# Performance work log

Hardware: AMD Instinct MI355X
Metric: run time of the kernel (lower is better)

The kernel has to match this reference:

```python
import jax, jax.numpy as jnp
import numpy as np

B, S, HID = 2, 2048, 2048
H, HK, D = 32, 8, 64
N_REP = H // HK
SCALE = D ** -0.5


def setup_inputs() -> dict:
    key = jax.random.key(0)
    ks = jax.random.split(key, 9)
    std = HID ** -0.5
    causal = jnp.tril(jnp.ones((S, S), dtype=bool))
    attention_mask = jnp.where(causal, 0.0, -1e9).astype(jnp.float32)[None, None]  # [1,1,S,S]
    return {
        "hidden_states": jax.random.normal(ks[0], (B, S, HID), jnp.float32),
        "attention_mask": attention_mask,
        "q_w": jax.random.normal(ks[1], (HID, H * D), jnp.float32) * std,
        "q_b": jax.random.normal(ks[2], (H * D,), jnp.float32) * 0.01,
        "k_w": jax.random.normal(ks[3], (HID, HK * D), jnp.float32) * std,
        "k_b": jax.random.normal(ks[4], (HK * D,), jnp.float32) * 0.01,
        "v_w": jax.random.normal(ks[5], (HID, HK * D), jnp.float32) * std,
        "v_b": jax.random.normal(ks[6], (HK * D,), jnp.float32) * 0.01,
        "dense_w": jax.random.normal(ks[7], (HID, HID), jnp.float32) * std,
        "dense_b": jax.random.normal(ks[8], (HID,), jnp.float32) * 0.01,
    }


def reference(hidden_states, attention_mask, q_w, q_b, k_w, k_b, v_w, v_b, dense_w, dense_b):
    b, s, _ = hidden_states.shape
    # projections -> [b, h, s, d]
    q = (hidden_states @ q_w + q_b).reshape(b, s, H, D).transpose(0, 2, 1, 3)
    k = (hidden_states @ k_w + k_b).reshape(b, s, HK, D).transpose(0, 2, 1, 3)
    v = (hidden_states @ v_w + v_b).reshape(b, s, HK, D).transpose(0, 2, 1, 3)
    # GQA: repeat_kv (repeat_interleave along head dim)
    k = jnp.repeat(k, N_REP, axis=1)  # [b, H, s, d]
    v = jnp.repeat(v, N_REP, axis=1)
    # eager attention: full score matrix
    scores = jnp.einsum("bhqd,bhkd->bhqk", q, k) * SCALE + attention_mask
    w = jax.nn.softmax(scores.astype(jnp.float32), axis=-1).astype(q.dtype)
    attn = jnp.einsum("bhqk,bhkd->bhqd", w, v)
    attn = attn.transpose(0, 2, 1, 3).reshape(b, s, H * D)
    return attn @ dense_w + dense_b
```

## Files before the change

### kernel.cpp

```cpp
#include <hip/hip_runtime.h>
#include <hip/hip_bf16.h>


typedef short s16x8 __attribute__((ext_vector_type(8)));
typedef float f32x4 __attribute__((ext_vector_type(4)));

static constexpr int BB = 2, SS = 2048, HID = 2048, HH = 32, HKV = 8, DD = 64;
static constexpr int MM = BB * SS;
static constexpr int NQKV = 3072;

#define DEV __device__ __forceinline__

DEV short f2bf(float f) {
    unsigned u = __builtin_bit_cast(unsigned, f);
    return (short)((u + 0x7fffu + ((u >> 16) & 1u)) >> 16);
}

DEV void stage16(const short* gsrc, short* lbase) {
    __builtin_amdgcn_global_load_lds((const __attribute__((address_space(1))) void*)gsrc,
                                     (__attribute__((address_space(3))) void*)lbase, 16, 0, 0);
}

__global__ __launch_bounds__(256) void cvt_f32_bf16(const float* __restrict__ in,
                                                    short* __restrict__ out, int n) {
    int i = (blockIdx.x * 256 + threadIdx.x) * 8;
    if (i >= n) return;
    float4 a = *reinterpret_cast<const float4*>(in + i);
    float4 b = *reinterpret_cast<const float4*>(in + i + 4);
    s16x8 o;
    o[0] = f2bf(a.x); o[1] = f2bf(a.y); o[2] = f2bf(a.z); o[3] = f2bf(a.w);
    o[4] = f2bf(b.x); o[5] = f2bf(b.y); o[6] = f2bf(b.z); o[7] = f2bf(b.w);
    *reinterpret_cast<s16x8*>(out + i) = o;
}

__global__ __launch_bounds__(256) void transpose_cvt(const float* __restrict__ in,
                                                     short* __restrict__ out,
                                                     int K, int N) {
    __shared__ float tile[32][33];
    int k0 = blockIdx.x * 32, n0 = blockIdx.y * 32;
    int tx = threadIdx.x & 31, ty = threadIdx.x >> 5;
#pragma unroll
    for (int r = ty; r < 32; r += 8)
        tile[r][tx] = in[(size_t)(k0 + r) * N + n0 + tx];
    __syncthreads();
#pragma unroll
    for (int r = ty; r < 32; r += 8)
        out[(size_t)(n0 + r) * K + k0 + tx] = f2bf(tile[tx][r]);
}

__global__ __launch_bounds__(256) void transpose_v(const short* __restrict__ QKV,
                                                   short* __restrict__ Vtg) {
    __shared__ int tile[32][33];
    const int s0 = blockIdx.x * 32, c0 = blockIdx.y * 32, b = blockIdx.z;
    const int tx = threadIdx.x & 31, ty = threadIdx.x >> 5;
#pragma unroll
    for (int r = ty; r < 32; r += 8)
        tile[r][tx] = QKV[(size_t)(b * SS + s0 + r) * NQKV + 2560 + c0 + tx];
    __syncthreads();
#pragma unroll
    for (int r = ty; r < 32; r += 8) {
        const int c = c0 + r;
        Vtg[((size_t)(b * HKV + (c >> 6)) * 64 + (c & 63)) * SS + s0 + tx] = (short)tile[tx][r];
    }
}

__global__ __launch_bounds__(256) void concat_bias(const float* __restrict__ qb,
                                                   const float* __restrict__ kb,
                                                   const float* __restrict__ vb,
                                                   float* __restrict__ cb) {
    int i = blockIdx.x * 256 + threadIdx.x;
    if (i < 2048) cb[i] = qb[i];
    else if (i < 2560) cb[i] = kb[i - 2048];
    else if (i < 3072) cb[i] = vb[i - 2560];
}

template <int BM, int BN, typename OutT>
__global__ __launch_bounds__(512) void gemm8p(const short* __restrict__ A,
                                              const short* __restrict__ Bt,
                                              const float* __restrict__ bias,
                                              OutT* __restrict__ C,
                                              int M, int N, int K, int qcols) {
    constexpr int NREP = BN / 64;
    constexpr int LA = BM / 128, LB = BN / 128;
    constexpr int W = LA + LB;
    __shared__ __align__(16) short lds[(BM + BN) * 128];
    const int tid = threadIdx.x, lane = tid & 63, wid = tid >> 6;
    const int fr = lane & 15, fk = lane >> 4;
    const int wm = wid >> 2, wn = wid & 3;
    const int nbn = N / BN;
    const int cpx = gridDim.x >> 3;
    const int wg = (blockIdx.x & 7) * cpx + (blockIdx.x >> 3);
    const int bm = wg / nbn, bn = wg % nbn;
    const int NT = K / 64;

    const short* Ablk = A + (size_t)bm * BM * K;
    const short* Bblk = Bt + (size_t)bn * BN * K;

    auto abase = [&](int bf, int kh) { return bf * (BM * 64) + kh * (BM * 32); };
    auto bbase = [&](int bf, int kh) { return 2 * (BM * 64) + bf * (BN * 64) + kh * (BN * 32); };

    auto stA = [&](int bf, int kh, int kt) {
#pragma unroll
        for (int l = 0; l < LA; ++l) {
            const int c = l * 512 + tid;
            const int r = c >> 2, sg = (c & 3) ^ ((r >> 1) & 3);
            stage16(Ablk + (size_t)r * K + kt + kh * 32 + sg * 8,
                    &lds[abase(bf, kh) + (l * 512 + wid * 64) * 8]);
        }
    };
    auto stB = [&](int bf, int kh, int kt) {
#pragma unroll
        for (int l = 0; l < LB; ++l) {
            const int c = l * 512 + tid;
            const int r = c >> 2, sg = (c & 3) ^ ((r >> 1) & 3);
            stage16(Bblk + (size_t)r * K + kt + kh * 32 + sg * 8,
                    &lds[bbase(bf, kh) + (l * 512 + wid * 64) * 8]);
        }
    };

    f32x4 acc[8][NREP] = {};

    stA(0, 0, 0); stB(0, 0, 0); stA(0, 1, 0); stB(0, 1, 0);
    asm volatile("s_waitcnt vmcnt(%0)" :: "n"(W) : "memory");
    __builtin_amdgcn_s_barrier();

    for (int t = 0; t < NT; ++t) {
        const int bf = t & 1, sf = bf ^ 1;
        const int ktn = (t + 1) * 64;
        const bool pf = (t + 1 < NT);
        s16x8 bfrag[NREP];
#pragma unroll
        for (int p = 0; p < 4; ++p) {
            const int ks = p >> 1, mh = p & 1;
            if (mh == 0) {
#pragma unroll
                for (int n = 0; n < NREP; ++n) {
                    const int row = wn * (BN / 4) + n * 16 + fr;
                    bfrag[n] = *reinterpret_cast<const s16x8*>(
                        &lds[bbase(bf, ks) + row * 32 + ((fk ^ ((row >> 1) & 3)) * 8)]);
                }
            }
            s16x8 afrag[4];
#pragma unroll
            for (int i = 0; i < 4; ++i) {
                const int row = wm * (BM / 2) + (mh * 4 + i) * 16 + fr;
                afrag[i] = *reinterpret_cast<const s16x8*>(
                    &lds[abase(bf, ks) + row * 32 + ((fk ^ ((row >> 1) & 3)) * 8)]);
            }
            if (pf) {
                if (p == 0) stA(sf, 0, ktn);
                else if (p == 1) stB(sf, 0, ktn);
                else if (p == 2) stA(sf, 1, ktn);
                else stB(sf, 1, ktn);
            }
            __builtin_amdgcn_s_barrier();
            asm volatile("s_waitcnt lgkmcnt(0)" ::: "memory");
            __builtin_amdgcn_sched_barrier(0);
            __builtin_amdgcn_s_setprio(1);
#pragma unroll
            for (int i = 0; i < 4; ++i)
#pragma unroll
                for (int n = 0; n < NREP; ++n)
                    acc[mh * 4 + i][n] = __builtin_amdgcn_mfma_f32_16x16x32_bf16(
                        afrag[i], bfrag[n], acc[mh * 4 + i][n], 0, 0, 0);
            __builtin_amdgcn_s_setprio(0);
            if (p == 1) {
                if (pf) asm volatile("s_waitcnt vmcnt(%0)" :: "n"(W) : "memory");
                else    asm volatile("s_waitcnt vmcnt(0)" ::: "memory");
            } else if (p == 3) {
                if (pf) asm volatile("s_waitcnt vmcnt(%0)" :: "n"(W) : "memory");
            }
            __builtin_amdgcn_s_barrier();
        }
    }

#pragma unroll
    for (int n = 0; n < NREP; ++n) {
        const int col = bn * BN + wn * (BN / 4) + n * 16 + fr;
        const float bv = bias[col];
        const float sc = (col < qcols) ? 0.125f : 1.0f;
#pragma unroll
        for (int mi = 0; mi < 8; ++mi) {
            const int row0 = bm * BM + wm * (BM / 2) + mi * 16 + fk * 4;
#pragma unroll
            for (int r = 0; r < 4; ++r) {
                const float v = (acc[mi][n][r] + bv) * sc;
                if constexpr (sizeof(OutT) == 2)
                    reinterpret_cast<short*>(C)[(size_t)(row0 + r) * N + col] = f2bf(v);
                else
                    reinterpret_cast<float*>(C)[(size_t)(row0 + r) * N + col] = v;
            }
        }
    }
}

__global__ __launch_bounds__(256, 2) void attn_fwd(
        const short* __restrict__ QKV,
        const short* __restrict__ Vtg,
        short* __restrict__ Ob) {
    constexpr int KB = 64;
    __shared__ __align__(16) short Qs[128 * 64];
    __shared__ __align__(16) short Ks[2][KB * 64];
    __shared__ __align__(16) short Vt[2][64 * 64];
    __shared__ __align__(16) short Ps[128 * 64];

    const int pair = blockIdx.x;
    const int bh = blockIdx.y;
    const int b = bh >> 5, h = bh & 31;
    const int kvh = h >> 2;
    const int tid = threadIdx.x, lane = tid & 63, wid = tid >> 6;
    const int fr = lane & 15, fk = lane >> 4;
    const int wq0 = wid * 32;

    const short* kbase = QKV + (size_t)b * SS * NQKV + 2048 + kvh * DD;
    const short* vbase = Vtg + (size_t)(b * HKV + kvh) * 64 * SS;

    auto stageKV = [&](int bb, int kv0) {
#pragma unroll
        for (int is = 0; is < 2; ++is) {
            const int c = is * 256 + wid * 64 + lane;
            const int r = c >> 3, sg = (c & 7) ^ (r & 7);
            stage16(kbase + (size_t)(kv0 + r) * NQKV + sg * 8,
                    &Ks[bb][(is * 256 + wid * 64) * 8]);
            stage16(vbase + (size_t)r * SS + kv0 + sg * 8,
                    &Vt[bb][(is * 256 + wid * 64) * 8]);
        }
    };
    auto stageQ = [&](int q0) {
        const short* qbase = QKV + ((size_t)b * SS + q0) * NQKV + h * DD;
#pragma unroll
        for (int is = 0; is < 4; ++is) {
            const int c = is * 256 + wid * 64 + lane;
            const int r = c >> 3, sg = (c & 7) ^ (r & 7);
            stage16(qbase + (size_t)r * NQKV + sg * 8,
                    &Qs[(is * 256 + wid * 64) * 8]);
        }
    };

    s16x8 ones = {};
    if (fr == 0) {
#pragma unroll
        for (int e = 0; e < 8; ++e) ones[e] = (short)0x3F80;
    }

    int cur = 0;
    stageQ(pair * 128);
    stageKV(0, 0);

    for (int sidx = 0; sidx < 2; ++sidx) {
        const int strip = sidx ? (15 - pair) : pair;
        const int q0 = strip * 128;
        const size_t qrow0 = (size_t)b * SS + q0;
        const int nt = 2 * strip + 2;

        __syncthreads();

        s16x8 aq[2][2];
#pragma unroll
        for (int i = 0; i < 2; ++i)
#pragma unroll
            for (int ks = 0; ks < 2; ++ks) {
                const int row = wq0 + i * 16 + fr;
                const int byte = (ks * 64 + fk * 16) ^ ((row & 7) << 4);
                aq[i][ks] = *reinterpret_cast<const s16x8*>(
                    reinterpret_cast<const char*>(Qs) + row * 128 + byte);
            }

        f32x4 acc_o[2][4] = {};
        f32x4 acc_l[2] = {};

        for (int t = 0; t < nt; ++t) {
            const int kv0 = t * KB;
            if (t + 1 < nt) {
                stageKV(cur ^ 1, kv0 + KB);
            } else if (sidx == 0) {
                stageQ((15 - pair) * 128);
                stageKV(cur ^ 1, 0);
            }

            f32x4 sacc[2][4] = {};
            __builtin_amdgcn_s_setprio(1);
#pragma unroll
            for (int j = 0; j < 4; ++j)
#pragma unroll
                for (int ks = 0; ks < 2; ++ks) {
                    const int row = j * 16 + fr;
                    const int byte = (ks * 64 + fk * 16) ^ ((row & 7) << 4);
                    s16x8 bk = *reinterpret_cast<const s16x8*>(
                        reinterpret_cast<const char*>(Ks[cur]) + row * 128 + byte);
#pragma unroll
                    for (int i = 0; i < 2; ++i)
                        sacc[i][j] = __builtin_amdgcn_mfma_f32_16x16x32_bf16(aq[i][ks], bk, sacc[i][j], 0, 0, 0);
                }
            __builtin_amdgcn_s_setprio(0);

            if (kv0 + KB - 1 > q0 + wq0) {
#pragma unroll
                for (int i = 0; i < 2; ++i) {
                    const int qg = q0 + wq0 + i * 16 + fk * 4;
#pragma unroll
                    for (int j = 0; j < 4; ++j) {
                        const int kvc = kv0 + j * 16 + fr;
#pragma unroll
                        for (int r = 0; r < 4; ++r)
                            if (kvc > qg + r) sacc[i][j][r] = -INFINITY;
                    }
                }
            }

#pragma unroll
            for (int i = 0; i < 2; ++i)
#pragma unroll
                for (int j = 0; j < 4; ++j)
#pragma unroll
                    for (int r = 0; r < 4; ++r) {
                        const int row = wq0 + i * 16 + fk * 4 + r;
                        const int byte = ((j * 16 + fr) * 2) ^ ((row & 7) << 4);
                        *reinterpret_cast<short*>(reinterpret_cast<char*>(Ps) + row * 128 + byte) =
                            f2bf(__expf(sacc[i][j][r]));
                    }

            s16x8 ap[2][2];
#pragma unroll
            for (int i = 0; i < 2; ++i)
#pragma unroll
                for (int ks = 0; ks < 2; ++ks) {
                    const int row = wq0 + i * 16 + fr;
                    const int byte = (ks * 64 + fk * 16) ^ ((row & 7) << 4);
                    ap[i][ks] = *reinterpret_cast<const s16x8*>(
                        reinterpret_cast<const char*>(Ps) + row * 128 + byte);
                }

            __builtin_amdgcn_s_setprio(1);
#pragma unroll
            for (int jd = 0; jd < 4; ++jd)
#pragma unroll
                for (int ks = 0; ks < 2; ++ks) {
                    const int row = jd * 16 + fr;
                    const int byte = (ks * 64 + fk * 16) ^ ((row & 7) << 4);
                    s16x8 bv = *reinterpret_cast<const s16x8*>(
                        reinterpret_cast<const char*>(Vt[cur]) + row * 128 + byte);
#pragma unroll
                    for (int i = 0; i < 2; ++i)
                        acc_o[i][jd] = __builtin_amdgcn_mfma_f32_16x16x32_bf16(ap[i][ks], bv, acc_o[i][jd], 0, 0, 0);
                }
#pragma unroll
            for (int i = 0; i < 2; ++i)
#pragma unroll
                for (int ks = 0; ks < 2; ++ks)
                    acc_l[i] = __builtin_amdgcn_mfma_f32_16x16x32_bf16(ap[i][ks], ones, acc_l[i], 0, 0, 0);
            __builtin_amdgcn_s_setprio(0);

            __syncthreads();
            cur ^= 1;
        }

#pragma unroll
        for (int i = 0; i < 2; ++i)
#pragma unroll
            for (int r = 0; r < 4; ++r) {
                const float l = __shfl(acc_l[i][r], (lane & 48));
                const float inv = 1.f / l;
                const size_t grow = (qrow0 + wq0 + i * 16 + fk * 4 + r) * (size_t)(HH * DD) + h * DD;
#pragma unroll
                for (int jd = 0; jd < 4; ++jd)
                    Ob[grow + jd * 16 + fr] = f2bf(acc_o[i][jd][r] * inv);
            }
    }
}

extern "C" void kernel_launch(void* const* d_in, const int* in_sizes, int n_in,
                              void* d_out, int out_size, void* d_ws, size_t ws_size,
                              hipStream_t stream) {
    const float* hidden  = (const float*)d_in[0];
    const float* q_w     = (const float*)d_in[2];
    const float* q_b     = (const float*)d_in[3];
    const float* k_w     = (const float*)d_in[4];
    const float* k_b     = (const float*)d_in[5];
    const float* v_w     = (const float*)d_in[6];
    const float* v_b     = (const float*)d_in[7];
    const float* dense_w = (const float*)d_in[8];
    const float* dense_b = (const float*)d_in[9];
    float* out = (float*)d_out;

    short* wt   = (short*)d_ws;
    short* dwt  = wt + 6291456;
    short* QKV  = dwt + 4194304;
    short* Vtg  = QKV + 12582912;
    short* hidb = Vtg + 2097152;
    short* Ob   = hidb;
    float* cbias = (float*)(hidb + 8388608);

    cvt_f32_bf16<<<4096, 256, 0, stream>>>(hidden, hidb, MM * HID);
    transpose_cvt<<<dim3(64, 64), 256, 0, stream>>>(q_w, wt, HID, HH * DD);
    transpose_cvt<<<dim3(64, 16), 256, 0, stream>>>(k_w, wt + 2048 * 2048, HID, HKV * DD);
    transpose_cvt<<<dim3(64, 16), 256, 0, stream>>>(v_w, wt + 2560 * 2048, HID, HKV * DD);
    transpose_cvt<<<dim3(64, 64), 256, 0, stream>>>(dense_w, dwt, HID, HID);
    concat_bias<<<12, 256, 0, stream>>>(q_b, k_b, v_b, cbias);

    gemm8p<256, 256, short><<<192, 512, 0, stream>>>(hidb, wt, cbias, QKV, MM, NQKV, HID, 2048);

    transpose_v<<<dim3(64, 16, 2), 256, 0, stream>>>(QKV, Vtg);

    attn_fwd<<<dim3(8, 64), 256, 0, stream>>>(QKV, Vtg, Ob);

    gemm8p<256, 128, float><<<256, 512, 0, stream>>>(Ob, dwt, dense_b, out, MM, HID, HID, 0);
}
```

Baseline: 199.2 us.

## Restructure GEMM pipeline to two phases per k-tile and retile QKV to 256x192

The GEMM main loop drops from four barrier-separated phases per k-tile to two. Each phase loads all 8 A fragments, interleaves the A and B prefetch issues between two MFMA halves, and uses per-wave vmcnt waits so it needs one barrier instead of two. The QKV projection switches from 256x256 tiles on 192 blocks to 256x192 tiles on 256 blocks to fill more CUs, so some threads issue an uneven number of B loads. This adds register pressure from holding 8 A fragments and relies on exact vmcnt bookkeeping for correctness.

Result: faster. 188.5 us (-5.4%).

```diff
diff --git a/kernel.cpp b/kernel.cpp
--- a/kernel.cpp
+++ b/kernel.cpp
@@ -80,9 +80,11 @@
                                               const float* __restrict__ bias,
                                               OutT* __restrict__ C,
                                               int M, int N, int K, int qcols) {
-    constexpr int NREP = BN / 64;
-    constexpr int LA = BM / 128, LB = BN / 128;
-    constexpr int W = LA + LB;
+    constexpr int NR = BN / 64;
+    constexpr int ACH = BM * 4;
+    constexpr int BCH = BN * 4;
+    static_assert(ACH % 512 == 0, "A chunks per half must be thread-uniform");
+    constexpr int SA = ACH / 512;
     __shared__ __align__(16) short lds[(BM + BN) * 128];
     const int tid = threadIdx.x, lane = tid & 63, wid = tid >> 6;
     const int fr = lane & 15, fk = lane >> 4;
@@ -101,7 +103,7 @@
 
     auto stA = [&](int bf, int kh, int kt) {
 #pragma unroll
-        for (int l = 0; l < LA; ++l) {
+        for (int l = 0; l < SA; ++l) {
             const int c = l * 512 + tid;
             const int r = c >> 2, sg = (c & 3) ^ ((r >> 1) & 3);
             stage16(Ablk + (size_t)r * K + kt + kh * 32 + sg * 8,
@@ -109,79 +111,89 @@
         }
     };
     auto stB = [&](int bf, int kh, int kt) {
-#pragma unroll
-        for (int l = 0; l < LB; ++l) {
-            const int c = l * 512 + tid;
+        {
+            const int c = tid;
             const int r = c >> 2, sg = (c & 3) ^ ((r >> 1) & 3);
             stage16(Bblk + (size_t)r * K + kt + kh * 32 + sg * 8,
-                    &lds[bbase(bf, kh) + (l * 512 + wid * 64) * 8]);
+                    &lds[bbase(bf, kh) + (wid * 64) * 8]);
+        }
+        if constexpr (BCH > 512) {
+            if (tid < BCH - 512) {
+                const int c = 512 + tid;
+                const int r = c >> 2, sg = (c & 3) ^ ((r >> 1) & 3);
+                stage16(Bblk + (size_t)r * K + kt + kh * 32 + sg * 8,
+                        &lds[bbase(bf, kh) + ((512 + wid * 64)) * 8]);
+            }
         }
     };
 
-    f32x4 acc[8][NREP] = {};
-
-    stA(0, 0, 0); stB(0, 0, 0); stA(0, 1, 0); stB(0, 1, 0);
-    asm volatile("s_waitcnt vmcnt(%0)" :: "n"(W) : "memory");
-    __builtin_amdgcn_s_barrier();
+    auto waithalf = [&](bool pf) {
+        if (!pf) { asm volatile("s_waitcnt vmcnt(0)" ::: "memory"); return; }
+        if constexpr (BCH > 512) {
+            if (wid < (BCH - 512) / 64) asm volatile("s_waitcnt vmcnt(4)" ::: "memory");
+            else                        asm volatile("s_waitcnt vmcnt(3)" ::: "memory");
+        } else {
+            asm volatile("s_waitcnt vmcnt(3)" ::: "memory");
+        }
+    };
+
+    f32x4 acc[8][NR] = {};
+
+    stA(0, 0, 0); stB(0, 0, 0);
+    stA(0, 1, 0); stB(0, 1, 0);
+    waithalf(true);
+    asm volatile("s_barrier" ::: "memory");
 
     for (int t = 0; t < NT; ++t) {
         const int bf = t & 1, sf = bf ^ 1;
         const int ktn = (t + 1) * 64;
         const bool pf = (t + 1 < NT);
-        s16x8 bfrag[NREP];
-#pragma unroll
-        for (int p = 0; p < 4; ++p) {
-            const int ks = p >> 1, mh = p & 1;
-            if (mh == 0) {
-#pragma unroll
-                for (int n = 0; n < NREP; ++n) {
-                    const int row = wn * (BN / 4) + n * 16 + fr;
-                    bfrag[n] = *reinterpret_cast<const s16x8*>(
-                        &lds[bbase(bf, ks) + row * 32 + ((fk ^ ((row >> 1) & 3)) * 8)]);
-                }
-            }
-            s16x8 afrag[4];
-#pragma unroll
-            for (int i = 0; i < 4; ++i) {
-                const int row = wm * (BM / 2) + (mh * 4 + i) * 16 + fr;
+#pragma unroll
+        for (int kh = 0; kh < 2; ++kh) {
+            s16x8 bfrag[NR], afrag[8];
+#pragma unroll
+            for (int n = 0; n < NR; ++n) {
+                const int row = wn * (BN / 4) + n * 16 + fr;
+                bfrag[n] = *reinterpret_cast<const s16x8*>(
+                    &lds[bbase(bf, kh) + row * 32 + ((fk ^ ((row >> 1) & 3)) * 8)]);
+            }
+#pragma unroll
+            for (int i = 0; i < 8; ++i) {
+                const int row = wm * 128 + i * 16 + fr;
                 afrag[i] = *reinterpret_cast<const s16x8*>(
-                    &lds[abase(bf, ks) + row * 32 + ((fk ^ ((row >> 1) & 3)) * 8)]);
-            }
-            if (pf) {
-                if (p == 0) stA(sf, 0, ktn);
-                else if (p == 1) stB(sf, 0, ktn);
-                else if (p == 2) stA(sf, 1, ktn);
-                else stB(sf, 1, ktn);
-            }
-            __builtin_amdgcn_s_barrier();
-            asm volatile("s_waitcnt lgkmcnt(0)" ::: "memory");
-            __builtin_amdgcn_sched_barrier(0);
+                    &lds[abase(bf, kh) + row * 32 + ((fk ^ ((row >> 1) & 3)) * 8)]);
+            }
+            if (pf) stA(sf, kh, ktn);
             __builtin_amdgcn_s_setprio(1);
 #pragma unroll
             for (int i = 0; i < 4; ++i)
 #pragma unroll
-                for (int n = 0; n < NREP; ++n)
-                    acc[mh * 4 + i][n] = __builtin_amdgcn_mfma_f32_16x16x32_bf16(
-                        afrag[i], bfrag[n], acc[mh * 4 + i][n], 0, 0, 0);
+                for (int n = 0; n < NR; ++n)
+                    acc[i][n] = __builtin_amdgcn_mfma_f32_16x16x32_bf16(
+                        afrag[i], bfrag[n], acc[i][n], 0, 0, 0);
             __builtin_amdgcn_s_setprio(0);
-            if (p == 1) {
-                if (pf) asm volatile("s_waitcnt vmcnt(%0)" :: "n"(W) : "memory");
-                else    asm volatile("s_waitcnt vmcnt(0)" ::: "memory");
-            } else if (p == 3) {
-                if (pf) asm volatile("s_waitcnt vmcnt(%0)" :: "n"(W) : "memory");
-            }
-            __builtin_amdgcn_s_barrier();
+            if (pf) stB(sf, kh, ktn);
+            __builtin_amdgcn_s_setprio(1);
+#pragma unroll
+            for (int i = 4; i < 8; ++i)
+#pragma unroll
+                for (int n = 0; n < NR; ++n)
+                    acc[i][n] = __builtin_amdgcn_mfma_f32_16x16x32_bf16(
+                        afrag[i], bfrag[n], acc[i][n], 0, 0, 0);
+            __builtin_amdgcn_s_setprio(0);
+            waithalf(pf);
+            asm volatile("s_barrier" ::: "memory");
         }
     }
 
 #pragma unroll
-    for (int n = 0; n < NREP; ++n) {
+    for (int n = 0; n < NR; ++n) {
         const int col = bn * BN + wn * (BN / 4) + n * 16 + fr;
         const float bv = bias[col];
         const float sc = (col < qcols) ? 0.125f : 1.0f;
 #pragma unroll
         for (int mi = 0; mi < 8; ++mi) {
-            const int row0 = bm * BM + wm * (BM / 2) + mi * 16 + fk * 4;
+            const int row0 = bm * BM + wm * 128 + mi * 16 + fk * 4;
 #pragma unroll
             for (int r = 0; r < 4; ++r) {
                 const float v = (acc[mi][n][r] + bv) * sc;
@@ -398,7 +410,7 @@
     transpose_cvt<<<dim3(64, 64), 256, 0, stream>>>(dense_w, dwt, HID, HID);
     concat_bias<<<12, 256, 0, stream>>>(q_b, k_b, v_b, cbias);
 
-    gemm8p<256, 256, short><<<192, 512, 0, stream>>>(hidb, wt, cbias, QKV, MM, NQKV, HID, 2048);
+    gemm8p<256, 192, short><<<256, 512, 0, stream>>>(hidb, wt, cbias, QKV, MM, NQKV, HID, 2048);
 
     transpose_v<<<dim3(64, 16, 2), 256, 0, stream>>>(QKV, Vtg);
 
```
